# Kernel tuning notes

Hardware: AMD Instinct MI355X
Metric: run time of the kernel (lower is better)

The kernel has to match this reference:

```python
import jax, jax.numpy as jnp
import numpy as np

EMBED_DIM = 512
NUM_HEADS = 8
HEAD_DIM = EMBED_DIM // NUM_HEADS
GRID = 48
BATCH = 8


def _locality_bias(grid_h, grid_w):
    # normalised negative squared L2 distances between patch centres, in [-1, 0]
    gy, gx = jnp.meshgrid(jnp.linspace(0.0, 1.0, grid_h),
                          jnp.linspace(0.0, 1.0, grid_w), indexing='ij')
    coords = jnp.stack([gy.reshape(-1), gx.reshape(-1)], axis=-1)  # (N, 2)
    diff = coords[None, :, :] - coords[:, None, :]                 # (N, N, 2)
    dist2 = jnp.sum(diff * diff, axis=-1)                          # (N, N)
    return -dist2 / jnp.max(dist2)


def setup_inputs() -> dict:
    key = jax.random.key(0)
    k_x, k_qkv, k_pw, k_pb, k_t, k_lw = jax.random.split(key, 6)
    N = GRID * GRID
    x = jax.random.normal(k_x, (BATCH, N, EMBED_DIM), dtype=jnp.float32)
    # torch nn.Linear weights are (out_features, in_features)
    qkv_w = jax.random.normal(k_qkv, (3 * EMBED_DIM, EMBED_DIM), dtype=jnp.float32) * 0.02
    proj_w = jax.random.normal(k_pw, (EMBED_DIM, EMBED_DIM), dtype=jnp.float32) * 0.02
    proj_b = jax.random.normal(k_pb, (EMBED_DIM,), dtype=jnp.float32) * 0.02
    init_temp = float(np.log(HEAD_DIM ** (-0.5)))
    temperature = init_temp + 0.02 * jax.random.normal(k_t, (NUM_HEADS, 1, 1), dtype=jnp.float32)
    locality_weight = 0.1 + 0.02 * jax.random.normal(k_lw, (NUM_HEADS,), dtype=jnp.float32)
    return {
        'x': x,
        'qkv_w': qkv_w,
        'proj_w': proj_w,
        'proj_b': proj_b,
        'temperature': temperature,
        'locality_weight': locality_weight,
        'grid_h': GRID,
        'grid_w': GRID,
    }


def reference(x, qkv_w, proj_w, proj_b, temperature, locality_weight, grid_h, grid_w):
    B, N, C = x.shape
    H = temperature.shape[0]
    D = C // H
    # qkv projection (no bias): (B, N, 3C) -> (3, B, H, N, D)
    qkv = (x @ qkv_w.T).reshape(B, N, 3, H, D)
    qkv = jnp.transpose(qkv, (2, 0, 3, 1, 4))
    q, k, v = qkv[0], qkv[1], qkv[2]              # each (B, H, N, D)
    scale = jnp.exp(temperature)                  # (H, 1, 1) learnable per-head temp
    attn = jnp.einsum('bhqd,bhkd->bhqk', q, k) * scale[None]
    loc = _locality_bias(grid_h, grid_w)          # (N, N), values in [-1, 0]
    attn = attn + locality_weight[None, :, None, None] * loc[None, None]
    attn = jax.nn.softmax(attn, axis=-1)          # dropout is identity (p=0 / eval)
    out = jnp.einsum('bhqk,bhkd->bhqd', attn, v)  # (B, H, N, D)
    out = jnp.transpose(out, (0, 2, 1, 3)).reshape(B, N, C)
    return out @ proj_w.T + proj_b
```

## Files before the change

### kernel.cpp

```cpp
#include <hip/hip_runtime.h>

typedef unsigned int   uint_ma   __attribute__((may_alias));
typedef unsigned short ushort_ma __attribute__((may_alias));
typedef float          float_ma  __attribute__((may_alias));
typedef __bf16 bf16x8 __attribute__((ext_vector_type(8)));
typedef float f32x4 __attribute__((ext_vector_type(4)));
typedef uint_ma u32x4 __attribute__((ext_vector_type(4)));
typedef ushort_ma u16x4 __attribute__((ext_vector_type(4)));

#define BATCH 8
#define NTOK 2304
#define CDIM 512
#define NH 8
#define HD 64
#define MROWS (BATCH * NTOK)
#define LOG2E 1.44269504088896f

constexpr size_t N_X  = (size_t)BATCH * NTOK * CDIM;
constexpr size_t N_WQ = (size_t)3 * CDIM * CDIM;
constexpr size_t N_WP = (size_t)CDIM * CDIM;
constexpr size_t OFF_XO = 0;
constexpr size_t OFF_WQ = OFF_XO + N_X;
constexpr size_t OFF_WP = OFF_WQ + N_WQ;
constexpr size_t OFF_Q  = OFF_WP + N_WP;
constexpr size_t OFF_K  = OFF_Q + N_X;
constexpr size_t OFF_V  = OFF_K + N_X;
constexpr size_t CV8 = (N_X + N_WQ + N_WP) / 8;

__device__ __forceinline__ float bf2f(unsigned short h) {
  unsigned int u = ((unsigned int)h) << 16;
  return __builtin_bit_cast(float, u);
}
__device__ __forceinline__ unsigned short f2bf(float f) {
  unsigned int u = __builtin_bit_cast(unsigned int, f);
  u += 0x7fffu + ((u >> 16) & 1u);
  return (unsigned short)(u >> 16);
}

__device__ __forceinline__ void gload16(const void* g, void* l) {
  __builtin_amdgcn_global_load_lds(
      (const __attribute__((address_space(1))) void*)g,
      (__attribute__((address_space(3))) void*)l, 16, 0, 0);
}

__global__ __launch_bounds__(256) void convert3(
    const float* __restrict__ s0, const float* __restrict__ s1,
    const float* __restrict__ s2, ushort_ma* __restrict__ base) {
  const size_t gid = (size_t)blockIdx.x * blockDim.x + threadIdx.x;
  const size_t stride = (size_t)gridDim.x * blockDim.x;
  for (size_t i = gid; i < CV8; i += stride) {
    size_t r = i;
    const float* src;
    size_t doff;
    if (r < N_X / 8) { src = s0; doff = OFF_XO; }
    else if ((r -= N_X / 8) < N_WQ / 8) { src = s1; doff = OFF_WQ; }
    else { r -= N_WQ / 8; src = s2; doff = OFF_WP; }
    const f32x4* fw = (const f32x4*)(src + r * 8);
    const f32x4 a = fw[0], b = fw[1];
    u16x4 lo, hi;
#pragma unroll
    for (int j = 0; j < 4; j++) { lo[j] = f2bf(a[j]); hi[j] = f2bf(b[j]); }
    ushort_ma* dst = base + doff + r * 8;
    *(u16x4*)dst = lo;
    *(u16x4*)(dst + 4) = hi;
  }
}

template <int MODE>
__global__ __launch_bounds__(256, 2) void gemm_bt(
    const ushort_ma* __restrict__ A, const ushort_ma* __restrict__ W,
    const float* __restrict__ aux,
    unsigned short* __restrict__ o0,
    unsigned short* __restrict__ o1,
    unsigned short* __restrict__ o2)
{
  __shared__ __align__(16) ushort_ma As[2][128][32];
  __shared__ __align__(16) ushort_ma Bs[2][128][32];
  const int K = CDIM;
  const int m0 = blockIdx.x * 128;
  const int n0 = blockIdx.y * 128;
  const int t = threadIdx.x;
  const int lane = t & 63;
  const int w = t >> 6;
  const int wm = (w >> 1) * 64, wn = (w & 1) * 64;
  const int lr = lane & 15, lq = lane >> 4;

  const int srow = w * 16 + (lane >> 2);
  const int scg = (lane & 3) ^ ((srow >> 1) & 3);
  const ushort_ma* Ag0 = A + (size_t)(m0 + srow) * K + scg * 8;
  const ushort_ma* Ag1 = Ag0 + (size_t)64 * K;
  const ushort_ma* Bg0 = W + (size_t)(n0 + srow) * K + scg * 8;
  const ushort_ma* Bg1 = Bg0 + (size_t)64 * K;

  const f32x4 fz = {0.f, 0.f, 0.f, 0.f};
  f32x4 acc[4][4];
#pragma unroll
  for (int i = 0; i < 4; i++)
#pragma unroll
    for (int j = 0; j < 4; j++) acc[i][j] = fz;

  auto issue = [&](int kt, int buf) {
    const int k0 = kt * 32;
    gload16(Ag0 + k0, (void*)&As[buf][w * 16][0]);
    gload16(Ag1 + k0, (void*)&As[buf][64 + w * 16][0]);
    gload16(Bg0 + k0, (void*)&Bs[buf][w * 16][0]);
    gload16(Bg1 + k0, (void*)&Bs[buf][64 + w * 16][0]);
  };

  issue(0, 0);
  const int colf = 8 * (lq ^ ((lr >> 1) & 3));

  for (int kt = 0; kt < 16; kt++) {
    const int buf = kt & 1;
    __syncthreads();
    if (kt < 15) issue(kt + 1, buf ^ 1);
    bf16x8 af[4], bfr[4];
#pragma unroll
    for (int i = 0; i < 4; i++)
      af[i] = __builtin_bit_cast(bf16x8, *(const u32x4*)(&As[buf][wm + i * 16 + lr][colf]));
#pragma unroll
    for (int j = 0; j < 4; j++)
      bfr[j] = __builtin_bit_cast(bf16x8, *(const u32x4*)(&Bs[buf][wn + j * 16 + lr][colf]));
#pragma unroll
    for (int i = 0; i < 4; i++)
#pragma unroll
      for (int j = 0; j < 4; j++)
        acc[i][j] = __builtin_amdgcn_mfma_f32_16x16x32_bf16(af[i], bfr[j], acc[i][j], 0, 0, 0);
  }

  if (MODE == 0) {
#pragma unroll
    for (int j = 0; j < 4; j++) {
      const int gc = n0 + wn + j * 16 + lr;
      const int which = gc >> 9;
      const int h = (gc >> 6) & 7;
      const int d = gc & 63;
#pragma unroll
      for (int i = 0; i < 4; i++) {
        const int gm0 = m0 + wm + i * 16 + lq * 4;
        const int b = gm0 / NTOK;
        const int np = gm0 - b * NTOK;
        if (which == 2) {
          u16x4 pk;
#pragma unroll
          for (int r = 0; r < 4; r++) pk[r] = f2bf(acc[i][j][r]);
          *(u16x4*)(o2 + ((size_t)((b * NH + h) * HD + d)) * NTOK + np) = pk;
        } else {
          const float sc = (which == 0) ? __expf(aux[h]) * LOG2E : 1.0f;
          unsigned short* dst = (which == 0) ? o0 : o1;
          const size_t base = ((size_t)((b * NH + h) * NTOK + np)) * HD + d;
#pragma unroll
          for (int r = 0; r < 4; r++) dst[base + (size_t)r * HD] = f2bf(acc[i][j][r] * sc);
        }
      }
    }
  } else {
    float_ma* outf = (float_ma*)o0;
#pragma unroll
    for (int j = 0; j < 4; j++) {
      const int gc = n0 + wn + j * 16 + lr;
      const float bv = aux[gc];
#pragma unroll
      for (int i = 0; i < 4; i++) {
        const int gm0 = m0 + wm + i * 16 + lq * 4;
#pragma unroll
        for (int r = 0; r < 4; r++)
          outf[(size_t)(gm0 + r) * CDIM + gc] = acc[i][j][r] + bv;
      }
    }
  }
}

__global__ __launch_bounds__(256, 3) void attn_kernel(
    const ushort_ma* __restrict__ Qg,
    const ushort_ma* __restrict__ Kg,
    const ushort_ma* __restrict__ Vg,
    const float* __restrict__ lwp,
    unsigned short* __restrict__ Og)
{
  __shared__ __align__(16) ushort_ma Ks[128][96];
  __shared__ __align__(16) ushort_ma Vs[64][136];
  __shared__ __align__(16) ushort_ma Ps[4][32][40];

  const int bh = blockIdx.y;
  const int b = bh >> 3, h = bh & 7;
  const int q0 = blockIdx.x * 128;
  const int t = threadIdx.x;
  const int lane = t & 63;
  const int w = t >> 6;
  const int lr = lane & 15, lq = lane >> 4;

  if (t < 128) {
    const u32x4 z4 = {0u, 0u, 0u, 0u};
    *(u32x4*)(&Ks[t][72]) = z4;
    *(u32x4*)(&Ks[t][80]) = z4;
    *(u32x4*)(&Ks[t][88]) = z4;
  }
  {
    const ushort_ma* Qb = Qg + ((size_t)bh * NTOK + q0) * HD;
#pragma unroll
    for (int it = 0; it < 4; it++) {
      const int q = t + it * 256;
      const int row = q >> 3, seg = (q & 7) * 8;
      *(u32x4*)(&Ks[row][seg]) = *(const u32x4*)(Qb + (size_t)row * HD + seg);
    }
  }
  __syncthreads();
  bf16x8 aQ[2][2];
#pragma unroll
  for (int mi = 0; mi < 2; mi++)
#pragma unroll
    for (int ks = 0; ks < 2; ks++)
      aQ[mi][ks] = __builtin_bit_cast(
          bf16x8, *(const u32x4*)(&Ks[w * 32 + mi * 16 + lr][ks * 32 + lq * 8]));

  const float cb2 = -0.5f * LOG2E * lwp[h];
  bf16x8 aQb[2];
#pragma unroll
  for (int mi = 0; mi < 2; mi++) {
    const int qrow = q0 + w * 32 + mi * 16 + lr;
    const int yy = qrow / 48;
    const int xx = qrow - yy * 48;
    const float fy = (float)yy * (1.0f / 47.0f);
    const float fx = (float)xx * (1.0f / 47.0f);
    u32x4 v = {0u, 0u, 0u, 0u};
    if (lq == 0) {
      v[0] = (unsigned int)f2bf(fy) | ((unsigned int)f2bf(fx) << 16);
      v[1] = (unsigned int)f2bf(fy * fy + fx * fx) | (0x3F80u << 16);
    }
    aQb[mi] = __builtin_bit_cast(bf16x8, v);
  }

  float l_i[8];
#pragma unroll
  for (int i = 0; i < 8; i++) l_i[i] = 0.0f;
  const f32x4 fz = {0.f, 0.f, 0.f, 0.f};
  f32x4 accO[2][4];
#pragma unroll
  for (int mi = 0; mi < 2; mi++)
#pragma unroll
    for (int nd = 0; nd < 4; nd++) accO[mi][nd] = fz;

  const ushort_ma* Kb = Kg + (size_t)bh * NTOK * HD;
  const ushort_ma* Vb = Vg + (size_t)bh * HD * NTOK;

  for (int kt = 0; kt < 18; kt++) {
    const int kv0 = kt * 128;
    __syncthreads();
    u32x4 kc[4], vc[4];
#pragma unroll
    for (int it = 0; it < 4; it++) {
      const int q = t + it * 256;
      kc[it] = *(const u32x4*)(Kb + (size_t)(kv0 + (q >> 3)) * HD + (q & 7) * 8);
      vc[it] = *(const u32x4*)(Vb + (size_t)(q >> 4) * NTOK + kv0 + (q & 15) * 8);
    }
#pragma unroll
    for (int it = 0; it < 4; it++) {
      const int q = t + it * 256;
      *(u32x4*)(&Ks[q >> 3][(q & 7) * 8]) = kc[it];
      *(u32x4*)(&Vs[q >> 4][(q & 15) * 8]) = vc[it];
    }
    if (t < 128) {
      const int kv = kv0 + t;
      const int yy = kv / 48;
      const int xx = kv - yy * 48;
      const float fy = (float)yy * (1.0f / 47.0f);
      const float fx = (float)xx * (1.0f / 47.0f);
      u32x4 bv;
      bv[0] = (unsigned int)f2bf(-2.0f * cb2 * fy) |
              ((unsigned int)f2bf(-2.0f * cb2 * fx) << 16);
      bv[1] = (unsigned int)f2bf(cb2) |
              ((unsigned int)f2bf(cb2 * (fy * fy + fx * fx)) << 16);
      bv[2] = 0u;
      bv[3] = 0u;
      *(u32x4*)(&Ks[t][64]) = bv;
    }
    __syncthreads();

#pragma unroll
    for (int c = 0; c < 4; c++) {
      f32x4 s2[2][2] = {{fz, fz}, {fz, fz}};
#pragma unroll
      for (int e2 = 0; e2 < 2; e2++) {
        const int ni = 2 * c + e2;
#pragma unroll
        for (int ks = 0; ks < 3; ks++) {
          const bf16x8 bK = __builtin_bit_cast(
              bf16x8, *(const u32x4*)(&Ks[ni * 16 + lr][ks * 32 + lq * 8]));
#pragma unroll
          for (int mi = 0; mi < 2; mi++) {
            const bf16x8 aOp = (ks < 2) ? aQ[mi][ks] : aQb[mi];
            s2[mi][e2] = __builtin_amdgcn_mfma_f32_16x16x32_bf16(aOp, bK, s2[mi][e2], 0, 0, 0);
          }
        }
      }
#pragma unroll
      for (int e2 = 0; e2 < 2; e2++) {
#pragma unroll
        for (int mi = 0; mi < 2; mi++)
#pragma unroll
          for (int r = 0; r < 4; r++) {
            const int ri = mi * 4 + r;
            const float p = __builtin_amdgcn_exp2f(s2[mi][e2][r]);
            const unsigned int pu = __builtin_bit_cast(unsigned int, p);
            l_i[ri] += __builtin_bit_cast(float, pu & 0xffff0000u);
            Ps[w][mi * 16 + lq * 4 + r][e2 * 16 + lr] = (unsigned short)(pu >> 16);
          }
      }
      __asm__ volatile("s_waitcnt lgkmcnt(0)" ::: "memory");
      bf16x8 aP[2];
#pragma unroll
      for (int mi = 0; mi < 2; mi++)
        aP[mi] = __builtin_bit_cast(
            bf16x8, *(const u32x4*)(&Ps[w][mi * 16 + lr][lq * 8]));
#pragma unroll
      for (int nd = 0; nd < 4; nd++) {
        const bf16x8 bV = __builtin_bit_cast(
            bf16x8, *(const u32x4*)(&Vs[nd * 16 + lr][c * 32 + lq * 8]));
#pragma unroll
        for (int mi = 0; mi < 2; mi++)
          accO[mi][nd] = __builtin_amdgcn_mfma_f32_16x16x32_bf16(aP[mi], bV, accO[mi][nd], 0, 0, 0);
      }
    }
  }

#pragma unroll
  for (int ri = 0; ri < 8; ri++) {
    float lv = l_i[ri];
    lv += __shfl_xor(lv, 1);
    lv += __shfl_xor(lv, 2);
    lv += __shfl_xor(lv, 4);
    lv += __shfl_xor(lv, 8);
    l_i[ri] = 1.0f / lv;
  }
#pragma unroll
  for (int mi = 0; mi < 2; mi++)
#pragma unroll
    for (int nd = 0; nd < 4; nd++)
#pragma unroll
      for (int r = 0; r < 4; r++) {
        const int np = q0 + w * 32 + mi * 16 + lq * 4 + r;
        Og[((size_t)(b * NTOK + np)) * CDIM + h * HD + nd * 16 + lr] =
            f2bf(accO[mi][nd][r] * l_i[mi * 4 + r]);
      }
}

extern "C" void kernel_launch(void* const* d_in, const int* in_sizes, int n_in,
                              void* d_out, int out_size, void* d_ws, size_t ws_size,
                              hipStream_t stream) {
  const float* x      = (const float*)d_in[0];
  const float* qkv_w  = (const float*)d_in[1];
  const float* proj_w = (const float*)d_in[2];
  const float* proj_b = (const float*)d_in[3];
  const float* temp   = (const float*)d_in[4];
  const float* lw     = (const float*)d_in[5];

  ushort_ma* base = (ushort_ma*)d_ws;
  ushort_ma* XB  = base + OFF_XO;
  ushort_ma* WQB = base + OFF_WQ;
  ushort_ma* WPB = base + OFF_WP;
  ushort_ma* Q   = base + OFF_Q;
  ushort_ma* Kt  = base + OFF_K;
  ushort_ma* Vt  = base + OFF_V;
  ushort_ma* O   = XB;

  convert3<<<1024, 256, 0, stream>>>(x, qkv_w, proj_w, base);
  gemm_bt<0><<<dim3(MROWS / 128, 1536 / 128), 256, 0, stream>>>(
      XB, WQB, temp, (unsigned short*)Q, (unsigned short*)Kt, (unsigned short*)Vt);
  attn_kernel<<<dim3(NTOK / 128, BATCH * NH), 256, 0, stream>>>(
      Q, Kt, Vt, lw, (unsigned short*)O);
  gemm_bt<1><<<dim3(MROWS / 128, CDIM / 128), 256, 0, stream>>>(
      O, WPB, proj_b, (unsigned short*)d_out, nullptr, nullptr);
}
```

Baseline: 311.6 us.

## Compute softmax row sums via MFMA with ones, swizzle P tile, tweak occupancy

Row sums of the softmax numerators are now accumulated with an extra MFMA against a ones vector instead of scalar adds and end-of-kernel shuffle reductions. The P scratch tile drops its padding and uses an XOR swizzle on the write and read indices to avoid LDS bank conflicts. The K tile padding changes from 96 to 104 columns, and the GEMM launch bounds raise target occupancy to 3 blocks per SM. The extra MFMAs add matrix-unit work per tile, and the higher GEMM occupancy target may constrain registers.

```diff
diff --git a/kernel.cpp b/kernel.cpp
--- a/kernel.cpp
+++ b/kernel.cpp
@@ -67,7 +67,7 @@
 }
 
 template <int MODE>
-__global__ __launch_bounds__(256, 2) void gemm_bt(
+__global__ __launch_bounds__(256, 3) void gemm_bt(
     const ushort_ma* __restrict__ A, const ushort_ma* __restrict__ W,
     const float* __restrict__ aux,
     unsigned short* __restrict__ o0,
@@ -178,9 +178,9 @@
     const float* __restrict__ lwp,
     unsigned short* __restrict__ Og)
 {
-  __shared__ __align__(16) ushort_ma Ks[128][96];
+  __shared__ __align__(16) ushort_ma Ks[128][104];
   __shared__ __align__(16) ushort_ma Vs[64][136];
-  __shared__ __align__(16) ushort_ma Ps[4][32][40];
+  __shared__ __align__(16) ushort_ma Ps[4][32][32];
 
   const int bh = blockIdx.y;
   const int b = bh >> 3, h = bh & 7;
@@ -231,15 +231,18 @@
     aQb[mi] = __builtin_bit_cast(bf16x8, v);
   }
 
-  float l_i[8];
-#pragma unroll
-  for (int i = 0; i < 8; i++) l_i[i] = 0.0f;
+  const u32x4 onesU = {0x3F803F80u, 0x3F803F80u, 0x3F803F80u, 0x3F803F80u};
+  const bf16x8 bOnes = __builtin_bit_cast(bf16x8, onesU);
+
   const f32x4 fz = {0.f, 0.f, 0.f, 0.f};
   f32x4 accO[2][4];
-#pragma unroll
-  for (int mi = 0; mi < 2; mi++)
+  f32x4 accL[2];
+#pragma unroll
+  for (int mi = 0; mi < 2; mi++) {
+    accL[mi] = fz;
 #pragma unroll
     for (int nd = 0; nd < 4; nd++) accO[mi][nd] = fz;
+  }
 
   const ushort_ma* Kb = Kg + (size_t)bh * NTOK * HD;
   const ushort_ma* Vb = Vg + (size_t)bh * HD * NTOK;
@@ -300,11 +303,11 @@
         for (int mi = 0; mi < 2; mi++)
 #pragma unroll
           for (int r = 0; r < 4; r++) {
-            const int ri = mi * 4 + r;
             const float p = __builtin_amdgcn_exp2f(s2[mi][e2][r]);
             const unsigned int pu = __builtin_bit_cast(unsigned int, p);
-            l_i[ri] += __builtin_bit_cast(float, pu & 0xffff0000u);
-            Ps[w][mi * 16 + lq * 4 + r][e2 * 16 + lr] = (unsigned short)(pu >> 16);
+            const int fw = (2 * lq + (r >> 1)) & 3;
+            const int gcol = 8 * ((e2 * 2 + (lr >> 3)) ^ fw) + (lr & 7);
+            Ps[w][mi * 16 + lq * 4 + r][gcol] = (unsigned short)(pu >> 16);
           }
       }
       __asm__ volatile("s_waitcnt lgkmcnt(0)" ::: "memory");
@@ -312,7 +315,8 @@
 #pragma unroll
       for (int mi = 0; mi < 2; mi++)
         aP[mi] = __builtin_bit_cast(
-            bf16x8, *(const u32x4*)(&Ps[w][mi * 16 + lr][lq * 8]));
+            bf16x8,
+            *(const u32x4*)(&Ps[w][mi * 16 + lr][8 * (lq ^ ((lr >> 1) & 3))]));
 #pragma unroll
       for (int nd = 0; nd < 4; nd++) {
         const bf16x8 bV = __builtin_bit_cast(
@@ -321,28 +325,26 @@
         for (int mi = 0; mi < 2; mi++)
           accO[mi][nd] = __builtin_amdgcn_mfma_f32_16x16x32_bf16(aP[mi], bV, accO[mi][nd], 0, 0, 0);
       }
-    }
-  }
-
-#pragma unroll
-  for (int ri = 0; ri < 8; ri++) {
-    float lv = l_i[ri];
-    lv += __shfl_xor(lv, 1);
-    lv += __shfl_xor(lv, 2);
-    lv += __shfl_xor(lv, 4);
-    lv += __shfl_xor(lv, 8);
-    l_i[ri] = 1.0f / lv;
-  }
-#pragma unroll
-  for (int mi = 0; mi < 2; mi++)
+#pragma unroll
+      for (int mi = 0; mi < 2; mi++)
+        accL[mi] = __builtin_amdgcn_mfma_f32_16x16x32_bf16(aP[mi], bOnes, accL[mi], 0, 0, 0);
+    }
+  }
+
+#pragma unroll
+  for (int mi = 0; mi < 2; mi++) {
+    f32x4 inv;
+#pragma unroll
+    for (int r = 0; r < 4; r++) inv[r] = 1.0f / accL[mi][r];
 #pragma unroll
     for (int nd = 0; nd < 4; nd++)
 #pragma unroll
       for (int r = 0; r < 4; r++) {
         const int np = q0 + w * 32 + mi * 16 + lq * 4 + r;
         Og[((size_t)(b * NTOK + np)) * CDIM + h * HD + nd * 16 + lr] =
-            f2bf(accO[mi][nd][r] * l_i[mi * 4 + r]);
-      }
+            f2bf(accO[mi][nd][r] * inv[r]);
+      }
+  }
 }
 
 extern "C" void kernel_launch(void* const* d_in, const int* in_sizes, int n_in,
```

Result: faster. 296.1 us (-5.0%).
